# Kernel optimization log

Measured on AMD Instinct MI355X. Metric: run time of the kernel, lower is better.

The kernel has to match this reference:

```python
import jax, jax.numpy as jnp
import numpy as np
import math

P_A = 0.5
MAX_SESSIONS = 400


def setup_inputs() -> dict:
    key = jax.random.key(0)
    B = 524288
    hist_p = jax.random.uniform(key, (B, MAX_SESSIONS), dtype=jnp.float32)
    return {"hist_p": hist_p}


def reference(hist_p) -> jnp.ndarray:
    B = hist_p.shape[0]
    # I_i is a ones vector in the original module, so I_i == 1.0 and I_i*6 == 6.0.
    I0 = jnp.ones((B,), dtype=hist_p.dtype)
    EF0 = jnp.full((B,), 2.5, dtype=hist_p.dtype)
    n0 = jnp.zeros((B,), dtype=hist_p.dtype)
    EF_floor = jnp.asarray(1.3, dtype=hist_p.dtype)

    def step(carry, p_i):
        I, EF, n = carry
        q = p_i * 5.0
        correct = q >= 3.0
        brk = p_i == -1.0
        # n==0, n==1, n>=2 partition the nonneg integer-valued n, so the
        # masked sum in the original equals a nested where-select.
        I_n = jnp.where(n >= 2.0, I * EF, jnp.where(n == 1.0, 6.0, 1.0))
        I_n = jnp.where(correct, I_n, 1.0)  # wrong answer resets interval to I_i = 1
        I = jnp.where(brk, I, I_n)
        I = jnp.clip(I, 1.0, 274.0)
        EF_n = EF + (0.1 - (5.0 - q) * (0.08 + (5.0 - q) * 0.02))
        EF_n = jnp.maximum(EF_n, EF_floor)
        EF = jnp.where(correct, EF_n, EF)
        n = (n + 1.0) * correct.astype(n.dtype)
        return (I, EF, n), None

    (I, EF, n), _ = jax.lax.scan(step, (I0, EF0, n0), hist_p.T)  # scan over 400 steps
    h_t = -I / math.log2(P_A)  # log2(0.5) = -1, so h_t = I
    return jnp.clip(h_t, 0.0001, 274.0)
```

## Files before the change

### kernel.cpp

```cpp
#include <hip/hip_runtime.h>


constexpr int T = 400;
constexpr int F4_PER_ROW = T / 4;
constexpr int CHUNK_F4 = 4;
constexpr int NCHUNK = F4_PER_ROW / CHUNK_F4;

__device__ __forceinline__ void sm2_step(float p, float& I, float& EF, float& n) {
    float q = p * 5.0f;
    bool correct = q >= 3.0f;
    bool brk = (p == -1.0f);
    float In = (n >= 2.0f) ? (I * EF) : ((n == 1.0f) ? 6.0f : 1.0f);
    In = correct ? In : 1.0f;
    I = brk ? I : In;
    I = fminf(fmaxf(I, 1.0f), 274.0f);
    float d = 5.0f - q;
    float EFn = EF + (0.1f - d * (0.08f + d * 0.02f));
    EFn = fmaxf(EFn, 1.3f);
    EF = correct ? EFn : EF;
    n = correct ? (n + 1.0f) : 0.0f;
}

__global__ __launch_bounds__(256) void sm2_kernel(const float* __restrict__ hist,
                                                  float* __restrict__ out, int B) {
    int row = blockIdx.x * blockDim.x + threadIdx.x;
    if (row >= B) return;

    const float4* rowp = reinterpret_cast<const float4*>(hist + (size_t)row * T);

    float I = 1.0f, EF = 2.5f, n = 0.0f;

    float4 cur[CHUNK_F4], nxt[CHUNK_F4];
#pragma unroll
    for (int j = 0; j < CHUNK_F4; ++j) cur[j] = rowp[j];

#pragma unroll 1
    for (int c = 0; c < NCHUNK; ++c) {
        int cn = (c + 1 < NCHUNK) ? (c + 1) : (NCHUNK - 1);
#pragma unroll
        for (int j = 0; j < CHUNK_F4; ++j) nxt[j] = rowp[cn * CHUNK_F4 + j];

#pragma unroll
        for (int j = 0; j < CHUNK_F4; ++j) {
            sm2_step(cur[j].x, I, EF, n);
            sm2_step(cur[j].y, I, EF, n);
            sm2_step(cur[j].z, I, EF, n);
            sm2_step(cur[j].w, I, EF, n);
        }

#pragma unroll
        for (int j = 0; j < CHUNK_F4; ++j) cur[j] = nxt[j];
    }

    out[row] = fminf(fmaxf(I, 0.0001f), 274.0f);
}

extern "C" void kernel_launch(void* const* d_in, const int* in_sizes, int n_in,
                              void* d_out, int out_size, void* d_ws, size_t ws_size,
                              hipStream_t stream) {
    const float* hist = (const float*)d_in[0];
    float* out = (float*)d_out;
    int B = in_sizes[0] / T;
    int threads = 256;
    int blocks = (B + threads - 1) / threads;
    sm2_kernel<<<blocks, threads, 0, stream>>>(hist, out, B);
}
```

Measured before the change: 1.062 ms.

## Stage row chunks through padded shared memory for coalesced global loads

```diff
diff --git a/kernel.cpp b/kernel.cpp
--- a/kernel.cpp
+++ b/kernel.cpp
@@ -2,9 +2,11 @@
 
 
 constexpr int T = 400;
-constexpr int F4_PER_ROW = T / 4;
-constexpr int CHUNK_F4 = 4;
-constexpr int NCHUNK = F4_PER_ROW / CHUNK_F4;
+constexpr int C = 40;
+constexpr int NCH = T / C;
+constexpr int F4 = C / 4;
+constexpr int BLK = 256;
+constexpr int PAD = 41;
 
 __device__ __forceinline__ void sm2_step(float p, float& I, float& EF, float& n) {
     float q = p * 5.0f;
@@ -21,38 +23,56 @@
     n = correct ? (n + 1.0f) : 0.0f;
 }
 
-__global__ __launch_bounds__(256) void sm2_kernel(const float* __restrict__ hist,
+__global__ __launch_bounds__(BLK) void sm2_kernel(const float* __restrict__ hist,
                                                   float* __restrict__ out, int B) {
-    int row = blockIdx.x * blockDim.x + threadIdx.x;
-    if (row >= B) return;
+    __shared__ float tile[BLK * PAD];
 
-    const float4* rowp = reinterpret_cast<const float4*>(hist + (size_t)row * T);
+    const int t = threadIdx.x;
+    const size_t base = (size_t)blockIdx.x * BLK;
+    const float* gbase = hist + base * T;
 
     float I = 1.0f, EF = 2.5f, n = 0.0f;
+    float4 stg[F4];
 
-    float4 cur[CHUNK_F4], nxt[CHUNK_F4];
+    int roff[F4];
+    int loff[F4];
 #pragma unroll
-    for (int j = 0; j < CHUNK_F4; ++j) cur[j] = rowp[j];
+    for (int i = 0; i < F4; ++i) {
+        int f = i * BLK + t;
+        int r = f / F4, c4 = f % F4;
+        roff[i] = r * T + c4 * 4;
+        loff[i] = r * PAD + c4 * 4;
+    }
+
+#pragma unroll
+    for (int i = 0; i < F4; ++i)
+        stg[i] = *reinterpret_cast<const float4*>(gbase + roff[i]);
 
 #pragma unroll 1
-    for (int c = 0; c < NCHUNK; ++c) {
-        int cn = (c + 1 < NCHUNK) ? (c + 1) : (NCHUNK - 1);
+    for (int ch = 0; ch < NCH; ++ch) {
 #pragma unroll
-        for (int j = 0; j < CHUNK_F4; ++j) nxt[j] = rowp[cn * CHUNK_F4 + j];
+        for (int i = 0; i < F4; ++i) {
+            float* p = &tile[loff[i]];
+            p[0] = stg[i].x; p[1] = stg[i].y; p[2] = stg[i].z; p[3] = stg[i].w;
+        }
+        __syncthreads();
 
+        if (ch + 1 < NCH) {
+            const float* gc = gbase + (ch + 1) * C;
 #pragma unroll
-        for (int j = 0; j < CHUNK_F4; ++j) {
-            sm2_step(cur[j].x, I, EF, n);
-            sm2_step(cur[j].y, I, EF, n);
-            sm2_step(cur[j].z, I, EF, n);
-            sm2_step(cur[j].w, I, EF, n);
+            for (int i = 0; i < F4; ++i)
+                stg[i] = *reinterpret_cast<const float4*>(gc + roff[i]);
         }
 
+        const float* myrow = &tile[t * PAD];
 #pragma unroll
-        for (int j = 0; j < CHUNK_F4; ++j) cur[j] = nxt[j];
+        for (int j = 0; j < C; ++j)
+            sm2_step(myrow[j], I, EF, n);
+
+        __syncthreads();
     }
 
-    out[row] = fminf(fmaxf(I, 0.0001f), 274.0f);
+    out[base + t] = fminf(fmaxf(I, 0.0001f), 274.0f);
 }
 
 extern "C" void kernel_launch(void* const* d_in, const int* in_sizes, int n_in,
@@ -61,7 +81,6 @@
     const float* hist = (const float*)d_in[0];
     float* out = (float*)d_out;
     int B = in_sizes[0] / T;
-    int threads = 256;
-    int blocks = (B + threads - 1) / threads;
-    sm2_kernel<<<blocks, threads, 0, stream>>>(hist, out, B);
+    int blocks = B / BLK;
+    sm2_kernel<<<blocks, BLK, 0, stream>>>(hist, out, B);
 }
```

New measurement: 1.048 ms. No clear change (-1.4%).
